# Optimization experiments

Measured on AMD Instinct MI355X. Metric: run time of the kernel, lower is better.

The kernel has to match this reference:

```python
import jax, jax.numpy as jnp
import numpy as np

KH, KW = 3, 3
SH, SW = 1, 1
DH, DW = 1, 1
OFFSET_GROUPS = 1
WEIGHT_GROUPS = 1


def setup_inputs() -> dict:
    key = jax.random.key(0)
    k1, k2, k3, k4 = jax.random.split(key, 4)
    B, C, H, W = 8, 128, 64, 64
    F = 128
    x = jax.random.normal(k1, (B, C, H, W), dtype=jnp.float32)
    offset = jax.random.normal(k2, (B, OFFSET_GROUPS * 2 * KH * KW, H, W), dtype=jnp.float32)
    mask = jax.random.uniform(k3, (B, OFFSET_GROUPS * KH * KW, H, W), dtype=jnp.float32)
    weight = jax.random.normal(k4, (F, C // WEIGHT_GROUPS, KH, KW), dtype=jnp.float32) * 0.05
    return {"x": x, "offset": offset, "mask": mask, "weight": weight}


def _deform_conv2d(x, offset, mask, weight):
    B, C, H, W = x.shape
    F = weight.shape[0]
    Ho, Wo = offset.shape[2], offset.shape[3]
    KK = KH * KW
    og = OFFSET_GROUPS
    Cg = C // og

    # SAME padding (TF convention, symmetric-ish: extra pad at bottom/right)
    pad_h = max((Ho - 1) * SH + (KH - 1) * DH + 1 - H, 0)
    pad_w = max((Wo - 1) * SW + (KW - 1) * DW + 1 - W, 0)
    pad_t, pad_l = pad_h // 2, pad_w // 2

    # offsets laid out as [B, og, KK, (dy,dx), Ho, Wo]
    off = offset.reshape(B, og, KK, 2, Ho, Wo)
    dy, dx = off[:, :, :, 0], off[:, :, :, 1]  # [B, og, KK, Ho, Wo]

    ki, kj = jnp.meshgrid(jnp.arange(KH), jnp.arange(KW), indexing="ij")
    ki = ki.reshape(KK)
    kj = kj.reshape(KK)
    base_y = (jnp.arange(Ho) * SH - pad_t)[None, :] + (ki * DH)[:, None]  # [KK, Ho]
    base_x = (jnp.arange(Wo) * SW - pad_l)[None, :] + (kj * DW)[:, None]  # [KK, Wo]

    py = base_y[None, None, :, :, None].astype(x.dtype) + dy  # [B, og, KK, Ho, Wo]
    px = base_x[None, None, :, None, :].astype(x.dtype) + dx

    y0 = jnp.floor(py)
    x0 = jnp.floor(px)
    ly = py - y0  # fractional parts
    lx = px - x0
    hy = 1.0 - ly
    hx = 1.0 - lx
    y0i = y0.astype(jnp.int32)
    x0i = x0.astype(jnp.int32)

    xg = x.reshape(B, og, Cg, H * W)

    def gather_corner(yi, xi):
        valid = (yi >= 0) & (yi < H) & (xi >= 0) & (xi < W)  # [B, og, KK, Ho, Wo]
        yc = jnp.clip(yi, 0, H - 1)
        xc = jnp.clip(xi, 0, W - 1)
        flat = (yc * W + xc).reshape(B, og, 1, KK * Ho * Wo)
        vals = jnp.take_along_axis(xg, flat, axis=3).reshape(B, og, Cg, KK, Ho, Wo)
        return vals * valid[:, :, None].astype(x.dtype)

    v00 = gather_corner(y0i, x0i)
    v01 = gather_corner(y0i, x0i + 1)
    v10 = gather_corner(y0i + 1, x0i)
    v11 = gather_corner(y0i + 1, x0i + 1)

    w00 = (hy * hx)[:, :, None]
    w01 = (hy * lx)[:, :, None]
    w10 = (ly * hx)[:, :, None]
    w11 = (ly * lx)[:, :, None]
    sampled = v00 * w00 + v01 * w01 + v10 * w10 + v11 * w11  # [B, og, Cg, KK, Ho, Wo]

    # modulation mask: [B, og, KK, Ho, Wo]
    m = mask.reshape(B, og, KK, Ho, Wo)
    sampled = sampled * m[:, :, None]

    # grouped matmul (weight_groups=1 -> plain); columns ordered c*KK + kk, matching
    # weight [F, C, KH, KW] flattened.
    cols = sampled.reshape(B, C * KK, Ho, Wo)
    out = jnp.einsum("fk,bkhw->bfhw", weight.reshape(F, C // WEIGHT_GROUPS * KK), cols)
    return out


def reference(x, offset, mask, weight):
    return _deform_conv2d(x, offset, mask, weight)
```

## Files before the change

kernel.cpp:

```cpp
#include <hip/hip_runtime.h>
#include <hip/hip_bf16.h>

typedef __attribute__((ext_vector_type(8))) short bf16x8;
typedef __attribute__((ext_vector_type(4))) float f32x4;
typedef __attribute__((ext_vector_type(2))) float f32x2;
typedef unsigned int uint32;
typedef unsigned short ushort_t;
typedef __attribute__((ext_vector_type(4))) uint32 u32x4;

__device__ __forceinline__ ushort_t f2bf(float f) {
    unsigned int u = __float_as_uint(f);
    u = (u + 0x7FFFu + ((u >> 16) & 1u)) >> 16;
    return (ushort_t)u;
}

__device__ __forceinline__ uint32 cvt_pk_bf16(float lo, float hi) {
    uint32 r;
    asm("v_cvt_pk_bf16_f32 %0, %1, %2" : "=v"(r) : "v"(lo), "v"(hi));
    return r;
}

__device__ __forceinline__ void gload_lds16(const void* g, void* l) {
    __builtin_amdgcn_global_load_lds(
        (const __attribute__((address_space(1))) uint32*)g,
        (__attribute__((address_space(3))) uint32*)l, 16, 0, 0);
}

__global__ __launch_bounds__(256) void prep_all(const float* __restrict__ x,
                                                const float* __restrict__ w,
                                                ushort_t* __restrict__ xt,
                                                ushort_t* __restrict__ wT2) {
    int bi = blockIdx.x;
    int t = threadIdx.x;
    if (bi >= 4096) {
        int idx = (bi - 4096) * 256 + t;
        int j  = idx & 7;
        int p  = (idx >> 3) & 15;
        int lu = (idx >> 7) & 3;
        int ft = (idx >> 9) & 7;
        int ks = (idx >> 12) & 3;
        int tap = idx >> 14;
        int f = ft * 16 + p;
        int c = ks * 32 + lu * 8 + j;
        wT2[idx] = f2bf(w[((size_t)f * 128 + c) * 9 + tap]);
        return;
    }
    __shared__ float tile[32][33];
    int b = bi & 7;
    int r2 = bi >> 3;
    int wb = r2 & 1, cb = (r2 >> 1) & 3, y = r2 >> 3;
    int lw = t & 31, lc = t >> 5;
    #pragma unroll
    for (int pass = 0; pass < 4; ++pass) {
        int c = cb * 32 + lc + pass * 8;
        tile[lc + pass * 8][lw] = x[(((size_t)b * 128 + c) * 64 + y) * 64 + wb * 32 + lw];
    }
    __syncthreads();
    int cc = t & 31, xl = t >> 5;
    #pragma unroll
    for (int pass = 0; pass < 4; ++pass) {
        int xll = xl + pass * 8;
        int xx = wb * 32 + xll;
        int c = cb * 32 + cc;
        int c2 = (((c >> 3) ^ (xx & 7)) << 3) | (c & 7);
        xt[(((size_t)b * 64 + y) * 64 + xx) * 128 + c2] = f2bf(tile[cc][xll]);
    }
}

__device__ __forceinline__ bf16x8 interp4(u32x4 c0, u32x4 c1, u32x4 c2, u32x4 c3,
                                          f32x4 wv) {
    uint32 rr[4];
    #pragma unroll
    for (int i = 0; i < 4; ++i) {
        f32x2 a, s;
        uint32 u = c0[i];
        a.x = __uint_as_float(u << 16); a.y = __uint_as_float(u & 0xffff0000u);
        s = a * wv.x;
        u = c1[i];
        a.x = __uint_as_float(u << 16); a.y = __uint_as_float(u & 0xffff0000u);
        s += a * wv.y;
        u = c2[i];
        a.x = __uint_as_float(u << 16); a.y = __uint_as_float(u & 0xffff0000u);
        s += a * wv.z;
        u = c3[i];
        a.x = __uint_as_float(u << 16); a.y = __uint_as_float(u & 0xffff0000u);
        s += a * wv.w;
        rr[i] = cvt_pk_bf16(s.x, s.y);
    }
    u32x4 q = {rr[0], rr[1], rr[2], rr[3]};
    return __builtin_bit_cast(bf16x8, q);
}

__global__ __launch_bounds__(512, 2) void dcn_main(
    const float* __restrict__ offset, const float* __restrict__ mask,
    const ushort_t* __restrict__ xt, const ushort_t* __restrict__ wT2,
    float* __restrict__ out)
{
    __shared__ ushort_t xwin[5 * 64 * 128];
    __shared__ ushort_t Abuf[2][16384];
    __shared__ float  pws_l[9][64][4];
    __shared__ uint32 pos_l[9][64];

    int bi = blockIdx.x;
    int b = bi & 7, ho = bi >> 3;
    int t = threadIdx.x, lane = t & 63, wid = t >> 6;
    int strip = wid & 3, tg = wid >> 2;
    int p = lane & 15, lu = lane >> 4;
    int pix = strip * 16 + p;
    int row0 = min(max(ho - 2, 0), 59);

    const char* xgb = (const char*)xt + (size_t)b * (64 * 64 * 256);

    {
        const char* ws = xgb + ((size_t)row0 << 14);
        #pragma unroll
        for (int r = 0; r < 10; ++r)
            gload_lds16(ws + (r * 512 + t) * 16, (char*)xwin + (r * 512 + t) * 16);
        const ushort_t* s0 = wT2 + t * 8;
        #pragma unroll
        for (int r = 0; r < 4; ++r)
            gload_lds16(s0 + r * 4096, &Abuf[0][(r * 512 + t) * 8]);
    }
    for (int item = t; item < 576; item += 512) {
        int k = item >> 6, pi = item & 63;
        int ki = k / 3, kj = k - ki * 3;
        float dy = offset[(((size_t)b * 18 + 2 * k)     * 64 + ho) * 64 + pi];
        float dx = offset[(((size_t)b * 18 + 2 * k + 1) * 64 + ho) * 64 + pi];
        float m  = mask  [(((size_t)b * 9  + k)         * 64 + ho) * 64 + pi];
        float py = (float)(ho - 1 + ki) + dy;
        float px = (float)(pi - 1 + kj) + dx;
        float y0f = floorf(py), x0f = floorf(px);
        float ly = py - y0f, lx = px - x0f;
        float hy = 1.f - ly, hx = 1.f - lx;
        int y0 = (int)y0f, x0 = (int)x0f;
        int y1 = y0 + 1, x1 = x0 + 1;
        float vy0 = (y0 >= 0 && y0 < 64) ? 1.f : 0.f;
        float vy1 = (y1 >= 0 && y1 < 64) ? 1.f : 0.f;
        float vx0 = (x0 >= 0 && x0 < 64) ? 1.f : 0.f;
        float vx1 = (x1 >= 0 && x1 < 64) ? 1.f : 0.f;
        pws_l[k][pi][0] = hy * hx * m * vy0 * vx0;
        pws_l[k][pi][1] = hy * lx * m * vy0 * vx1;
        pws_l[k][pi][2] = ly * hx * m * vy1 * vx0;
        pws_l[k][pi][3] = ly * lx * m * vy1 * vx1;
        int y0c = min(max(y0, 0), 63), y1c = min(max(y1, 0), 63);
        int x0c = min(max(x0, 0), 63), x1c = min(max(x1, 0), 63);
        pos_l[k][pi] = (uint32)(y0c * 64 + x0c) | ((uint32)(y1c * 64 + x1c) << 16);
    }
    __syncthreads();

    f32x4 acc[8];
    #pragma unroll
    for (int i = 0; i < 8; ++i) acc[i] = (f32x4){0.f, 0.f, 0.f, 0.f};

    int cl = tg * 128 + lu * 16;

    #pragma unroll 1
    for (int tap = 0; tap < 9; ++tap) {
        if (tap < 8) {
            ushort_t* An = &Abuf[(tap + 1) & 1][0];
            const ushort_t* ss = wT2 + (size_t)(tap + 1) * 16384 + t * 8;
            #pragma unroll
            for (int r = 0; r < 4; ++r)
                gload_lds16(ss + r * 4096, &An[(r * 512 + t) * 8]);
        }

        uint32 pp = pos_l[tap][pix];
        f32x4 wv = *(const f32x4*)pws_l[tap][pix];
        int i00 = pp & 0xffffu, i11 = pp >> 16;
        int y0c = i00 >> 6, x0c = i00 & 63;
        int y1c = i11 >> 6, x1c = i11 & 63;

        u32x4 g[4][2];
        #pragma unroll
        for (int c = 0; c < 4; ++c) {
            int yc = (c < 2) ? y0c : y1c;
            int xc = (c & 1) ? x1c : x0c;
            int rl = yc - row0;
            int sw = (xc & 7) << 4;
            int o0 = cl ^ sw;
            int o1 = (cl + 64) ^ sw;
            bool inw = (unsigned)rl < 5u;
            const char* lp = (const char*)xwin + (inw ? ((rl * 64 + xc) << 8) : 0);
            g[c][0] = *(const u32x4*)(lp + o0);
            g[c][1] = *(const u32x4*)(lp + o1);
            if (!inw) {
                const char* gp = xgb + ((size_t)(yc * 64 + xc) << 8);
                g[c][0] = *(const u32x4*)(gp + o0);
                g[c][1] = *(const u32x4*)(gp + o1);
            }
        }

        bf16x8 b0 = interp4(g[0][0], g[1][0], g[2][0], g[3][0], wv);
        bf16x8 b1 = interp4(g[0][1], g[1][1], g[2][1], g[3][1], wv);

        const ushort_t* Ab = &Abuf[tap & 1][0];
        #pragma unroll
        for (int q = 0; q < 2; ++q) {
            int ks = tg * 2 + q;
            bf16x8 bb = q ? b1 : b0;
            #pragma unroll
            for (int ft = 0; ft < 8; ++ft) {
                bf16x8 aa = *(const bf16x8*)&Ab[((ks * 8 + ft) * 64 + lane) * 8];
                acc[ft] = __builtin_amdgcn_mfma_f32_16x16x32_bf16(aa, bb, acc[ft], 0, 0, 0);
            }
        }

        __syncthreads();
    }

    float* red = (float*)&Abuf[0][0];
    if (tg == 1) {
        #pragma unroll
        for (int ft = 0; ft < 8; ++ft)
            #pragma unroll
            for (int r = 0; r < 4; ++r) {
                int f = ft * 16 + lu * 4 + r;
                red[(strip * 128 + f) * 17 + p] = acc[ft][r];
            }
    }
    __syncthreads();
    if (tg == 0) {
        float* outb = out + (size_t)b * 128 * 4096 + ho * 64 + strip * 16 + p;
        #pragma unroll
        for (int ft = 0; ft < 8; ++ft)
            #pragma unroll
            for (int r = 0; r < 4; ++r) {
                int f = ft * 16 + lu * 4 + r;
                outb[(size_t)f * 4096] = acc[ft][r] + red[(strip * 128 + f) * 17 + p];
            }
    }
}

extern "C" void kernel_launch(void* const* d_in, const int* in_sizes, int n_in,
                              void* d_out, int out_size, void* d_ws, size_t ws_size,
                              hipStream_t stream) {
    const float* x      = (const float*)d_in[0];
    const float* offset = (const float*)d_in[1];
    const float* mask   = (const float*)d_in[2];
    const float* weight = (const float*)d_in[3];
    float* out = (float*)d_out;

    ushort_t* xt  = (ushort_t*)d_ws;
    ushort_t* wT2 = xt + (size_t)8 * 64 * 64 * 128;
    if (ws_size < (size_t)(8 * 64 * 64 * 128 + 9 * 16384) * 2) return;

    prep_all<<<4672, 256, 0, stream>>>(x, weight, xt, wT2);
    dcn_main<<<512, 512, 0, stream>>>(offset, mask, xt, wT2, out);
}
```

Before: 42.42 us.

## Split deform-conv block into 16 waves over K, filter and pixel groups

Blocks grow from 512 to 1024 threads. Each of the 16 waves now owns one K-slice of 32 channels, one half of the filters and 32 pixels, instead of 8 waves splitting only K in two. The weight operand is read straight from global memory in a new MFMA-ready layout, which removes the double-buffered LDS weight staging and the per-tap barriers. A three-stage LDS tree reduction across the four K-slices is added at the end. The intent is more waves to hide gather latency and less LDS and sync traffic, at the cost of redundant global weight loads and a longer final reduction.

```diff
diff --git a/kernel.cpp b/kernel.cpp
--- a/kernel.cpp
+++ b/kernel.cpp
@@ -29,20 +29,20 @@
 __global__ __launch_bounds__(256) void prep_all(const float* __restrict__ x,
                                                 const float* __restrict__ w,
                                                 ushort_t* __restrict__ xt,
-                                                ushort_t* __restrict__ wT2) {
+                                                ushort_t* __restrict__ wT4) {
     int bi = blockIdx.x;
     int t = threadIdx.x;
     if (bi >= 4096) {
         int idx = (bi - 4096) * 256 + t;
-        int j  = idx & 7;
-        int p  = (idx >> 3) & 15;
-        int lu = (idx >> 7) & 3;
-        int ft = (idx >> 9) & 7;
-        int ks = (idx >> 12) & 3;
-        int tap = idx >> 14;
-        int f = ft * 16 + p;
-        int c = ks * 32 + lu * 8 + j;
-        wT2[idx] = f2bf(w[((size_t)f * 128 + c) * 9 + tap]);
+        int j    = idx & 7;
+        int lane = (idx >> 3) & 63;
+        int ft   = (idx >> 9) & 3;
+        int fg   = (idx >> 11) & 1;
+        int ks   = (idx >> 12) & 3;
+        int tap  = idx >> 14;
+        int f = fg * 64 + ft * 16 + (lane & 15);
+        int c = ks * 32 + (lane >> 4) * 8 + j;
+        wT4[idx] = f2bf(w[((size_t)f * 128 + c) * 9 + tap]);
         return;
     }
     __shared__ float tile[32][33];
@@ -91,22 +91,20 @@
     return __builtin_bit_cast(bf16x8, q);
 }
 
-__global__ __launch_bounds__(512, 2) void dcn_main(
+__global__ __launch_bounds__(1024, 4) void dcn_main(
     const float* __restrict__ offset, const float* __restrict__ mask,
-    const ushort_t* __restrict__ xt, const ushort_t* __restrict__ wT2,
+    const ushort_t* __restrict__ xt, const ushort_t* __restrict__ wT4,
     float* __restrict__ out)
 {
     __shared__ ushort_t xwin[5 * 64 * 128];
-    __shared__ ushort_t Abuf[2][16384];
     __shared__ float  pws_l[9][64][4];
     __shared__ uint32 pos_l[9][64];
 
     int bi = blockIdx.x;
     int b = bi & 7, ho = bi >> 3;
     int t = threadIdx.x, lane = t & 63, wid = t >> 6;
-    int strip = wid & 3, tg = wid >> 2;
+    int pxg = wid & 1, fg = (wid >> 1) & 1, ks = wid >> 2;
     int p = lane & 15, lu = lane >> 4;
-    int pix = strip * 16 + p;
     int row0 = min(max(ho - 2, 0), 59);
 
     const char* xgb = (const char*)xt + (size_t)b * (64 * 64 * 256);
@@ -114,15 +112,11 @@
     {
         const char* ws = xgb + ((size_t)row0 << 14);
         #pragma unroll
-        for (int r = 0; r < 10; ++r)
-            gload_lds16(ws + (r * 512 + t) * 16, (char*)xwin + (r * 512 + t) * 16);
-        const ushort_t* s0 = wT2 + t * 8;
-        #pragma unroll
-        for (int r = 0; r < 4; ++r)
-            gload_lds16(s0 + r * 4096, &Abuf[0][(r * 512 + t) * 8]);
-    }
-    for (int item = t; item < 576; item += 512) {
-        int k = item >> 6, pi = item & 63;
+        for (int r = 0; r < 5; ++r)
+            gload_lds16(ws + (r * 1024 + t) * 16, (char*)xwin + (r * 1024 + t) * 16);
+    }
+    if (t < 576) {
+        int k = t >> 6, pi = t & 63;
         int ki = k / 3, kj = k - ki * 3;
         float dy = offset[(((size_t)b * 18 + 2 * k)     * 64 + ho) * 64 + pi];
         float dx = offset[(((size_t)b * 18 + 2 * k + 1) * 64 + ho) * 64 + pi];
@@ -148,87 +142,105 @@
     }
     __syncthreads();
 
-    f32x4 acc[8];
-    #pragma unroll
-    for (int i = 0; i < 8; ++i) acc[i] = (f32x4){0.f, 0.f, 0.f, 0.f};
-
-    int cl = tg * 128 + lu * 16;
+    f32x4 acc[4][2];
+    #pragma unroll
+    for (int i = 0; i < 4; ++i) {
+        acc[i][0] = (f32x4){0.f, 0.f, 0.f, 0.f};
+        acc[i][1] = (f32x4){0.f, 0.f, 0.f, 0.f};
+    }
+
+    int klu = ks * 64 + lu * 16;
 
     #pragma unroll 1
     for (int tap = 0; tap < 9; ++tap) {
-        if (tap < 8) {
-            ushort_t* An = &Abuf[(tap + 1) & 1][0];
-            const ushort_t* ss = wT2 + (size_t)(tap + 1) * 16384 + t * 8;
+        const ushort_t* ab = wT4 + (size_t)(((tap * 4 + ks) * 2 + fg) * 4) * 512 + lane * 8;
+
+        bf16x8 bt[2];
+        #pragma unroll
+        for (int tile = 0; tile < 2; ++tile) {
+            int px = pxg * 32 + tile * 16 + p;
+            uint32 pp = pos_l[tap][px];
+            f32x4 wv = *(const f32x4*)pws_l[tap][px];
+            int i00 = pp & 0xffffu, i11 = pp >> 16;
+            int y0c = i00 >> 6, x0c = i00 & 63;
+            int y1c = i11 >> 6, x1c = i11 & 63;
+            u32x4 g[4];
             #pragma unroll
-            for (int r = 0; r < 4; ++r)
-                gload_lds16(ss + r * 4096, &An[(r * 512 + t) * 8]);
+            for (int c = 0; c < 4; ++c) {
+                int yc = (c < 2) ? y0c : y1c;
+                int xc = (c & 1) ? x1c : x0c;
+                int rl = yc - row0;
+                int off = klu ^ ((xc & 7) << 4);
+                bool inw = (unsigned)rl < 5u;
+                const char* lp = (const char*)xwin + (((inw ? rl : 0) * 64 + xc) << 8) + off;
+                g[c] = *(const u32x4*)lp;
+                if (!inw) {
+                    const char* gp = xgb + (((size_t)yc * 64 + xc) << 8) + off;
+                    g[c] = *(const u32x4*)gp;
+                }
+            }
+            bt[tile] = interp4(g[0], g[1], g[2], g[3], wv);
         }
 
-        uint32 pp = pos_l[tap][pix];
-        f32x4 wv = *(const f32x4*)pws_l[tap][pix];
-        int i00 = pp & 0xffffu, i11 = pp >> 16;
-        int y0c = i00 >> 6, x0c = i00 & 63;
-        int y1c = i11 >> 6, x1c = i11 & 63;
-
-        u32x4 g[4][2];
-        #pragma unroll
-        for (int c = 0; c < 4; ++c) {
-            int yc = (c < 2) ? y0c : y1c;
-            int xc = (c & 1) ? x1c : x0c;
-            int rl = yc - row0;
-            int sw = (xc & 7) << 4;
-            int o0 = cl ^ sw;
-            int o1 = (cl + 64) ^ sw;
-            bool inw = (unsigned)rl < 5u;
-            const char* lp = (const char*)xwin + (inw ? ((rl * 64 + xc) << 8) : 0);
-            g[c][0] = *(const u32x4*)(lp + o0);
-            g[c][1] = *(const u32x4*)(lp + o1);
-            if (!inw) {
-                const char* gp = xgb + ((size_t)(yc * 64 + xc) << 8);
-                g[c][0] = *(const u32x4*)(gp + o0);
-                g[c][1] = *(const u32x4*)(gp + o1);
-            }
+        #pragma unroll
+        for (int ft = 0; ft < 4; ++ft) {
+            bf16x8 aa = *(const bf16x8*)(ab + ft * 512);
+            acc[ft][0] = __builtin_amdgcn_mfma_f32_16x16x32_bf16(aa, bt[0], acc[ft][0], 0, 0, 0);
+            acc[ft][1] = __builtin_amdgcn_mfma_f32_16x16x32_bf16(aa, bt[1], acc[ft][1], 0, 0, 0);
         }
-
-        bf16x8 b0 = interp4(g[0][0], g[1][0], g[2][0], g[3][0], wv);
-        bf16x8 b1 = interp4(g[0][1], g[1][1], g[2][1], g[3][1], wv);
-
-        const ushort_t* Ab = &Abuf[tap & 1][0];
-        #pragma unroll
-        for (int q = 0; q < 2; ++q) {
-            int ks = tg * 2 + q;
-            bf16x8 bb = q ? b1 : b0;
+    }
+
+    __syncthreads();
+    float* red = (float*)xwin;
+
+    #define DUMP(SLOT)                                                          \
+        do {                                                                    \
+            _Pragma("unroll")                                                   \
+            for (int ft = 0; ft < 4; ++ft)                                      \
+                _Pragma("unroll")                                               \
+                for (int tile = 0; tile < 2; ++tile)                            \
+                    _Pragma("unroll")                                           \
+                    for (int r = 0; r < 4; ++r)                                 \
+                        red[(SLOT) * 8192 + (fg * 64 + ft * 16 + lu * 4 + r) * 64 \
+                            + pxg * 32 + tile * 16 + p] = acc[ft][tile][r];     \
+        } while (0)
+    #define ADDIN(SLOT)                                                         \
+        do {                                                                    \
+            _Pragma("unroll")                                                   \
+            for (int ft = 0; ft < 4; ++ft)                                      \
+                _Pragma("unroll")                                               \
+                for (int tile = 0; tile < 2; ++tile)                            \
+                    _Pragma("unroll")                                           \
+                    for (int r = 0; r < 4; ++r)                                 \
+                        acc[ft][tile][r] += red[(SLOT) * 8192                   \
+                            + (fg * 64 + ft * 16 + lu * 4 + r) * 64             \
+                            + pxg * 32 + tile * 16 + p];                        \
+        } while (0)
+
+    if (ks == 1) DUMP(0);
+    if (ks == 3) DUMP(1);
+    __syncthreads();
+    if (ks == 0) ADDIN(0);
+    if (ks == 2) ADDIN(1);
+    __syncthreads();
+    if (ks == 2) DUMP(0);
+    __syncthreads();
+    if (ks == 0) {
+        ADDIN(0);
+        float* outb = out + (size_t)b * 128 * 4096 + ho * 64;
+        #pragma unroll
+        for (int ft = 0; ft < 4; ++ft)
             #pragma unroll
-            for (int ft = 0; ft < 8; ++ft) {
-                bf16x8 aa = *(const bf16x8*)&Ab[((ks * 8 + ft) * 64 + lane) * 8];
-                acc[ft] = __builtin_amdgcn_mfma_f32_16x16x32_bf16(aa, bb, acc[ft], 0, 0, 0);
-            }
-        }
-
-        __syncthreads();
-    }
-
-    float* red = (float*)&Abuf[0][0];
-    if (tg == 1) {
-        #pragma unroll
-        for (int ft = 0; ft < 8; ++ft)
-            #pragma unroll
-            for (int r = 0; r < 4; ++r) {
-                int f = ft * 16 + lu * 4 + r;
-                red[(strip * 128 + f) * 17 + p] = acc[ft][r];
-            }
-    }
-    __syncthreads();
-    if (tg == 0) {
-        float* outb = out + (size_t)b * 128 * 4096 + ho * 64 + strip * 16 + p;
-        #pragma unroll
-        for (int ft = 0; ft < 8; ++ft)
-            #pragma unroll
-            for (int r = 0; r < 4; ++r) {
-                int f = ft * 16 + lu * 4 + r;
-                outb[(size_t)f * 4096] = acc[ft][r] + red[(strip * 128 + f) * 17 + p];
-            }
-    }
+            for (int tile = 0; tile < 2; ++tile)
+                #pragma unroll
+                for (int r = 0; r < 4; ++r) {
+                    int f = fg * 64 + ft * 16 + lu * 4 + r;
+                    int px = pxg * 32 + tile * 16 + p;
+                    outb[(size_t)f * 4096 + px] = acc[ft][tile][r];
+                }
+    }
+    #undef DUMP
+    #undef ADDIN
 }
 
 extern "C" void kernel_launch(void* const* d_in, const int* in_sizes, int n_in,
@@ -241,9 +253,9 @@
     float* out = (float*)d_out;
 
     ushort_t* xt  = (ushort_t*)d_ws;
-    ushort_t* wT2 = xt + (size_t)8 * 64 * 64 * 128;
+    ushort_t* wT4 = xt + (size_t)8 * 64 * 64 * 128;
     if (ws_size < (size_t)(8 * 64 * 64 * 128 + 9 * 16384) * 2) return;
 
-    prep_all<<<4672, 256, 0, stream>>>(x, weight, xt, wT2);
-    dcn_main<<<512, 512, 0, stream>>>(offset, mask, xt, wT2, out);
-}
+    prep_all<<<4672, 256, 0, stream>>>(x, weight, xt, wT4);
+    dcn_main<<<512, 1024, 0, stream>>>(offset, mask, xt, wT4, out);
+}
```

Result: slower. 51.14 us (+20.5%).
